# Performance work log

Hardware: AMD Instinct MI355X
Metric: run time of the kernel (lower is better)

Reference implementation:

```python
import jax, jax.numpy as jnp
import numpy as np

B, N, D, H = 4, 2048, 1024, 16
HD = D // H

def setup_inputs() -> dict:
    key = jax.random.key(0)
    ks = jax.random.split(key, 5)
    s = 0.02
    return {
        "x": jax.random.normal(ks[0], (B, N, D), dtype=jnp.float32),
        "W_qkv": jax.random.normal(ks[1], (D, 3 * D), dtype=jnp.float32) * s,
        "b_qkv": jnp.zeros((3 * D,), dtype=jnp.float32),
        "W_proj": jax.random.normal(ks[2], (D, D), dtype=jnp.float32) * s,
        "b_proj": jnp.zeros((D,), dtype=jnp.float32),
    }

def reference(x, W_qkv, b_qkv, W_proj, b_proj):
    scale = HD ** -0.5
    qkv = x @ W_qkv + b_qkv                       # [B,N,3D]
    qkv = qkv.reshape(B, N, 3, H, HD).transpose(2, 0, 3, 1, 4)  # [3,B,H,N,hd]
    q, k, v = qkv[0], qkv[1], qkv[2]
    attn = jnp.einsum('bhqd,bhkd->bhqk', q, k) * scale
    attn = jax.nn.softmax(attn, axis=-1)
    out = jnp.einsum('bhqk,bhkd->bhqd', attn, v)  # [B,H,N,hd]
    out = out.transpose(0, 2, 1, 3).reshape(B, N, D)
    return out @ W_proj + b_proj
```

## Files before the change

kernel.cpp:

```cpp
#include <hip/hip_runtime.h>


typedef __bf16 bf8v  __attribute__((ext_vector_type(8)));
typedef __bf16 bf4v  __attribute__((ext_vector_type(4)));
typedef float  f32x4 __attribute__((ext_vector_type(4)));

typedef const __attribute__((address_space(1))) void* gptr_t;
typedef __attribute__((address_space(3))) void*       lptr_t;

#define GLL16(g, l) __builtin_amdgcn_global_load_lds((gptr_t)(g), (lptr_t)(l), 16, 0, 0)

#define MFMA_BF16_16x16x32 __builtin_amdgcn_mfma_f32_16x16x32_bf16

static constexpr int Bsz = 4, Nseq = 2048, Dmod = 1024, H = 16, HD = 64;
static constexpr int Mtok = Bsz * Nseq;

__global__ __launch_bounds__(256) void cast_f32_bf16(const float* __restrict__ in,
                                                     __bf16* __restrict__ out, int n4) {
    int i = blockIdx.x * blockDim.x + threadIdx.x;
    int stride = gridDim.x * blockDim.x;
    for (; i < n4; i += stride) {
        float4 f = reinterpret_cast<const float4*>(in)[i];
        bf4v o;
        o[0] = (__bf16)f.x; o[1] = (__bf16)f.y; o[2] = (__bf16)f.z; o[3] = (__bf16)f.w;
        reinterpret_cast<bf4v*>(out)[i] = o;
    }
}

__global__ __launch_bounds__(256) void transpose_cast(const float* __restrict__ W,
                                                      __bf16* __restrict__ WT,
                                                      int K, int N) {
    __shared__ float t[32][33];
    int tx = threadIdx.x, ty = threadIdx.y;
    int bx = blockIdx.x, by = blockIdx.y;
#pragma unroll
    for (int j = 0; j < 4; ++j) {
        int k = by * 32 + ty + j * 8;
        int n = bx * 32 + tx;
        t[ty + j * 8][tx] = W[(size_t)k * N + n];
    }
    __syncthreads();
#pragma unroll
    for (int j = 0; j < 4; ++j) {
        int n = bx * 32 + ty + j * 8;
        int k = by * 32 + tx;
        WT[(size_t)n * K + k] = (__bf16)t[tx][ty + j * 8];
    }
}

template <int EPI>
__global__ __launch_bounds__(256) void gemm_bt(const __bf16* __restrict__ A,
                                               const __bf16* __restrict__ Bt,
                                               const float* __restrict__ bias,
                                               float* __restrict__ Cf,
                                               __bf16* __restrict__ Qo,
                                               __bf16* __restrict__ Ko,
                                               __bf16* __restrict__ Vo,
                                               int M, int N, int K) {
    __shared__ __attribute__((aligned(16))) __bf16 As[128 * 32];
    __shared__ __attribute__((aligned(16))) __bf16 Bs[128 * 32];

    const int nwg = gridDim.x;
    const int wg = (blockIdx.x & 7) * (nwg >> 3) + (blockIdx.x >> 3);

    const int nbn = N >> 7;
    const int bm = wg / nbn, bn = wg % nbn;
    const int tid = threadIdx.x;
    const int w = tid >> 6, l = tid & 63;
    const int wr = w >> 1, wc = w & 1;

    const int lr = l >> 2;
    const int lk = (l & 3) * 8;
    const int fr = l & 15;
    const int fk = (l >> 4) * 8;

    f32x4 acc[4][4] = {};

    for (int k0 = 0; k0 < K; k0 += 32) {
        const int c0 = w, c1 = w + 4;
        GLL16(A  + (size_t)(bm * 128 + c0 * 16 + lr) * K + k0 + lk, &As[c0 * 512]);
        GLL16(A  + (size_t)(bm * 128 + c1 * 16 + lr) * K + k0 + lk, &As[c1 * 512]);
        GLL16(Bt + (size_t)(bn * 128 + c0 * 16 + lr) * K + k0 + lk, &Bs[c0 * 512]);
        GLL16(Bt + (size_t)(bn * 128 + c1 * 16 + lr) * K + k0 + lk, &Bs[c1 * 512]);
        __syncthreads();

        bf8v af[4], bf[4];
#pragma unroll
        for (int m = 0; m < 4; ++m)
            af[m] = *(const bf8v*)&As[(wr * 64 + m * 16 + fr) * 32 + fk];
#pragma unroll
        for (int n = 0; n < 4; ++n)
            bf[n] = *(const bf8v*)&Bs[(wc * 64 + n * 16 + fr) * 32 + fk];
#pragma unroll
        for (int m = 0; m < 4; ++m)
#pragma unroll
            for (int n = 0; n < 4; ++n)
                acc[m][n] = MFMA_BF16_16x16x32(af[m], bf[n], acc[m][n], 0, 0, 0);
        __syncthreads();
    }

    const int r0 = bm * 128 + wr * 64;
    const int c0 = bn * 128 + wc * 64;
#pragma unroll
    for (int m = 0; m < 4; ++m)
#pragma unroll
        for (int n = 0; n < 4; ++n)
#pragma unroll
            for (int r = 0; r < 4; ++r) {
                int row = r0 + m * 16 + (l >> 4) * 4 + r;
                int col = c0 + n * 16 + (l & 15);
                float v = acc[m][n][r] + bias[col];
                if (EPI == 0) {
                    int mat = col >> 10, rem = col & 1023;
                    int h = rem >> 6, hd = rem & 63;
                    int b = row >> 11, nt = row & 2047;
                    size_t dst = (((size_t)(b * H + h)) * Nseq + nt) * HD + hd;
                    __bf16 val = (__bf16)v;
                    if (mat == 0)      Qo[dst] = val;
                    else if (mat == 1) Ko[dst] = val;
                    else               Vo[dst] = val;
                } else {
                    Cf[(size_t)row * N + col] = v;
                }
            }
}

__global__ __launch_bounds__(256) void attn_kernel(const __bf16* __restrict__ Q,
                                                   const __bf16* __restrict__ K,
                                                   const __bf16* __restrict__ V,
                                                   __bf16* __restrict__ Ao) {
    __shared__ __attribute__((aligned(16))) __bf16 Ks[64 * 64];
    __shared__ __attribute__((aligned(16))) __bf16 Vt[64 * 72];
    __shared__ __attribute__((aligned(16))) __bf16 Pl[4][16 * 72];

    const int tid = threadIdx.x;
    const int w = tid >> 6, l = tid & 63;

    const int nwg = gridDim.x;
    const int id = (blockIdx.x & 7) * (nwg >> 3) + (blockIdx.x >> 3);
    const int qb = id & 31;
    const int h = (id >> 5) & 15;
    const int b = id >> 9;
    const size_t base = (size_t)(b * H + h) * Nseq * HD;

    const int fr = l & 15;
    const int fkh = (l >> 4) * 8;

    const int qrow = qb * 64 + w * 16 + fr;
    bf8v qf[2];
    qf[0] = *(const bf8v*)&Q[base + (size_t)qrow * HD + fkh];
    qf[1] = *(const bf8v*)&Q[base + (size_t)qrow * HD + 32 + fkh];
#pragma unroll
    for (int j = 0; j < 8; ++j) {
        qf[0][j] = (__bf16)((float)qf[0][j] * 0.125f);
        qf[1][j] = (__bf16)((float)qf[1][j] * 0.125f);
    }

    f32x4 o[4] = {};
    float psum[4] = {0.f, 0.f, 0.f, 0.f};

    for (int kt = 0; kt < Nseq / 64; ++kt) {
        __syncthreads();
#pragma unroll
        for (int i = 0; i < 2; ++i) {
            int c = i * 256 + tid;
            int r = c >> 3, part = c & 7;
            GLL16(K + base + (size_t)(kt * 64 + r) * HD + ((part ^ (r & 7)) << 3),
                  &Ks[(i * 256 + w * 64) * 8]);
        }
#pragma unroll
        for (int i = 0; i < 2; ++i) {
            int c = i * 256 + tid;
            int rowk = c >> 3, part = c & 7;
            bf8v v8 = *(const bf8v*)&V[base + (size_t)(kt * 64 + rowk) * HD + part * 8];
#pragma unroll
            for (int j = 0; j < 8; ++j) {
                int d = part * 8 + j;
                Vt[d * 72 + (rowk ^ (part << 3))] = v8[j];
            }
        }
        __syncthreads();

        f32x4 s[4];
#pragma unroll
        for (int st = 0; st < 4; ++st) {
            int krow = st * 16 + fr;
            int key = (krow & 7) << 3;
            bf8v kf0 = *(const bf8v*)&Ks[krow * 64 + (fkh ^ key)];
            bf8v kf1 = *(const bf8v*)&Ks[krow * 64 + ((fkh + 32) ^ key)];
            f32x4 a = {};
            a = MFMA_BF16_16x16x32(qf[0], kf0, a, 0, 0, 0);
            a = MFMA_BF16_16x16x32(qf[1], kf1, a, 0, 0, 0);
            s[st] = a;
        }

        float p[4][4];
#pragma unroll
        for (int st = 0; st < 4; ++st)
#pragma unroll
            for (int r = 0; r < 4; ++r) p[st][r] = __expf(s[st][r]);
#pragma unroll
        for (int r = 0; r < 4; ++r)
            psum[r] += (p[0][r] + p[1][r]) + (p[2][r] + p[3][r]);

#pragma unroll
        for (int st = 0; st < 4; ++st)
#pragma unroll
            for (int r = 0; r < 4; ++r) {
                int qr = (l >> 4) * 4 + r;
                int col = st * 16 + (l & 15);
                Pl[w][qr * 72 + (col ^ ((qr >> 2) << 3))] = (__bf16)p[st][r];
            }

        int pkey = (fr >> 2) << 3;
        bf8v pa0 = *(const bf8v*)&Pl[w][fr * 72 + (fkh ^ pkey)];
        bf8v pa1 = *(const bf8v*)&Pl[w][fr * 72 + ((fkh + 32) ^ pkey)];
#pragma unroll
        for (int t = 0; t < 4; ++t) {
            int drow = t * 16 + fr;
            int vkey = ((drow >> 3) & 7) << 3;
            bf8v vf0 = *(const bf8v*)&Vt[drow * 72 + (fkh ^ vkey)];
            bf8v vf1 = *(const bf8v*)&Vt[drow * 72 + ((fkh + 32) ^ vkey)];
            o[t] = MFMA_BF16_16x16x32(pa0, vf0, o[t], 0, 0, 0);
            o[t] = MFMA_BF16_16x16x32(pa1, vf1, o[t], 0, 0, 0);
        }
    }

    float inv[4];
#pragma unroll
    for (int r = 0; r < 4; ++r) {
        float ps = psum[r];
#pragma unroll
        for (int off = 1; off < 16; off <<= 1) ps += __shfl_xor(ps, off);
        inv[r] = 1.f / ps;
    }
#pragma unroll
    for (int t = 0; t < 4; ++t)
#pragma unroll
        for (int r = 0; r < 4; ++r) {
            int row = (l >> 4) * 4 + r;
            int nq = qb * 64 + w * 16 + row;
            int hd = t * 16 + (l & 15);
            Ao[((size_t)(b * Nseq + nq)) * Dmod + h * HD + hd] = (__bf16)(o[t][r] * inv[r]);
        }
}

extern "C" void kernel_launch(void* const* d_in, const int* in_sizes, int n_in,
                              void* d_out, int out_size, void* d_ws, size_t ws_size,
                              hipStream_t stream) {
    const float* x      = (const float*)d_in[0];
    const float* W_qkv  = (const float*)d_in[1];
    const float* b_qkv  = (const float*)d_in[2];
    const float* W_proj = (const float*)d_in[3];
    const float* b_proj = (const float*)d_in[4];
    float* out = (float*)d_out;

    char* ws = (char*)d_ws;
    __bf16* Xb     = (__bf16*)(ws);
    __bf16* WqkvT  = (__bf16*)(ws + 16777216);
    __bf16* WprojT = (__bf16*)(ws + 16777216 + 6291456);
    __bf16* Qb     = (__bf16*)(ws + 25165824);
    __bf16* Kb     = (__bf16*)(ws + 25165824 + 16777216);
    __bf16* Vb     = (__bf16*)(ws + 25165824 + 33554432);
    __bf16* Ab     = Xb;

    cast_f32_bf16<<<2048, 256, 0, stream>>>(x, Xb, Mtok * Dmod / 4);

    dim3 tb(32, 8);
    transpose_cast<<<dim3(3 * Dmod / 32, Dmod / 32), tb, 0, stream>>>(W_qkv, WqkvT, Dmod, 3 * Dmod);
    transpose_cast<<<dim3(Dmod / 32, Dmod / 32), tb, 0, stream>>>(W_proj, WprojT, Dmod, Dmod);

    gemm_bt<0><<<(Mtok / 128) * (3 * Dmod / 128), 256, 0, stream>>>(
        Xb, WqkvT, b_qkv, nullptr, Qb, Kb, Vb, Mtok, 3 * Dmod, Dmod);

    attn_kernel<<<Bsz * H * (Nseq / 64), 256, 0, stream>>>(Qb, Kb, Vb, Ab);

    gemm_bt<1><<<(Mtok / 128) * (Dmod / 128), 256, 0, stream>>>(
        Ab, WprojT, b_proj, out, nullptr, nullptr, nullptr, Mtok, Dmod, Dmod);
}
```

Baseline: 331.6 us.

## Write V transposed from QKV GEMM and double-buffer attention K/V tiles

The QKV GEMM epilogue now writes V in a head-dim-major (transposed) layout, so the attention kernel can load V tiles with direct global-to-LDS copies instead of an in-register scatter transpose. K and V tiles are double-buffered, with the next tile prefetched while the current one is computed, and waits use vmcnt plus raw barriers. Each workgroup now handles 128 query rows (32 per wave) so every K/V fragment read from LDS feeds twice as many MFMAs. In exchange the GEMM's V stores become strided along the sequence, which may hurt that epilogue, and the grid shrinks to half as many workgroups.

```diff
diff --git a/kernel.cpp b/kernel.cpp
--- a/kernel.cpp
+++ b/kernel.cpp
@@ -114,135 +114,155 @@
                     int mat = col >> 10, rem = col & 1023;
                     int h = rem >> 6, hd = rem & 63;
                     int b = row >> 11, nt = row & 2047;
-                    size_t dst = (((size_t)(b * H + h)) * Nseq + nt) * HD + hd;
                     __bf16 val = (__bf16)v;
-                    if (mat == 0)      Qo[dst] = val;
-                    else if (mat == 1) Ko[dst] = val;
-                    else               Vo[dst] = val;
+                    if (mat == 0)
+                        Qo[(((size_t)(b * H + h)) * Nseq + nt) * HD + hd] = val;
+                    else if (mat == 1)
+                        Ko[(((size_t)(b * H + h)) * Nseq + nt) * HD + hd] = val;
+                    else
+                        Vo[(((size_t)(b * H + h)) * HD + hd) * Nseq + nt] = val;
                 } else {
                     Cf[(size_t)row * N + col] = v;
                 }
             }
 }
 
-__global__ __launch_bounds__(256) void attn_kernel(const __bf16* __restrict__ Q,
-                                                   const __bf16* __restrict__ K,
-                                                   const __bf16* __restrict__ V,
-                                                   __bf16* __restrict__ Ao) {
-    __shared__ __attribute__((aligned(16))) __bf16 Ks[64 * 64];
-    __shared__ __attribute__((aligned(16))) __bf16 Vt[64 * 72];
-    __shared__ __attribute__((aligned(16))) __bf16 Pl[4][16 * 72];
+__global__ __launch_bounds__(256, 2) void attn_kernel(const __bf16* __restrict__ Q,
+                                                      const __bf16* __restrict__ K,
+                                                      const __bf16* __restrict__ VT,
+                                                      __bf16* __restrict__ Ao) {
+    __shared__ __attribute__((aligned(16))) __bf16 Ks[2][64 * 64];
+    __shared__ __attribute__((aligned(16))) __bf16 Vts[2][64 * 64];
+    __shared__ __attribute__((aligned(16))) __bf16 Pl[4][32 * 72];
 
     const int tid = threadIdx.x;
     const int w = tid >> 6, l = tid & 63;
 
     const int nwg = gridDim.x;
     const int id = (blockIdx.x & 7) * (nwg >> 3) + (blockIdx.x >> 3);
-    const int qb = id & 31;
-    const int h = (id >> 5) & 15;
-    const int b = id >> 9;
+    const int qb = id & 15;
+    const int h = (id >> 4) & 15;
+    const int b = id >> 8;
     const size_t base = (size_t)(b * H + h) * Nseq * HD;
 
     const int fr = l & 15;
     const int fkh = (l >> 4) * 8;
 
-    const int qrow = qb * 64 + w * 16 + fr;
-    bf8v qf[2];
-    qf[0] = *(const bf8v*)&Q[base + (size_t)qrow * HD + fkh];
-    qf[1] = *(const bf8v*)&Q[base + (size_t)qrow * HD + 32 + fkh];
-#pragma unroll
-    for (int j = 0; j < 8; ++j) {
-        qf[0][j] = (__bf16)((float)qf[0][j] * 0.125f);
-        qf[1][j] = (__bf16)((float)qf[1][j] * 0.125f);
-    }
-
-    f32x4 o[4] = {};
-    float psum[4] = {0.f, 0.f, 0.f, 0.f};
+    const int sr0 = tid >> 3, sp0 = tid & 7;
+    const int sr1 = (256 + tid) >> 3, sp1 = tid & 7;
+
+    bf8v qf[2][2];
+#pragma unroll
+    for (int m = 0; m < 2; ++m) {
+        const int qrow = qb * 128 + w * 32 + m * 16 + fr;
+        qf[m][0] = *(const bf8v*)&Q[base + (size_t)qrow * HD + fkh];
+        qf[m][1] = *(const bf8v*)&Q[base + (size_t)qrow * HD + 32 + fkh];
+#pragma unroll
+        for (int j = 0; j < 8; ++j) {
+            qf[m][0][j] = (__bf16)((float)qf[m][0][j] * 0.125f);
+            qf[m][1][j] = (__bf16)((float)qf[m][1][j] * 0.125f);
+        }
+    }
+
+    f32x4 o[2][4] = {};
+    f32x4 psum[2] = {};
+
+#define STAGE(buf, kt)                                                                   \
+    do {                                                                                 \
+        GLL16(K  + base + (size_t)((kt) * 64 + sr0) * HD + ((sp0 ^ (sr0 & 7)) << 3),     \
+              &Ks[buf][(w * 64) * 8]);                                                   \
+        GLL16(K  + base + (size_t)((kt) * 64 + sr1) * HD + ((sp1 ^ (sr1 & 7)) << 3),     \
+              &Ks[buf][(256 + w * 64) * 8]);                                             \
+        GLL16(VT + base + (size_t)sr0 * Nseq + (kt) * 64 + ((sp0 ^ (sr0 & 7)) << 3),     \
+              &Vts[buf][(w * 64) * 8]);                                                  \
+        GLL16(VT + base + (size_t)sr1 * Nseq + (kt) * 64 + ((sp1 ^ (sr1 & 7)) << 3),     \
+              &Vts[buf][(256 + w * 64) * 8]);                                            \
+    } while (0)
+
+    STAGE(0, 0);
 
     for (int kt = 0; kt < Nseq / 64; ++kt) {
-        __syncthreads();
-#pragma unroll
-        for (int i = 0; i < 2; ++i) {
-            int c = i * 256 + tid;
-            int r = c >> 3, part = c & 7;
-            GLL16(K + base + (size_t)(kt * 64 + r) * HD + ((part ^ (r & 7)) << 3),
-                  &Ks[(i * 256 + w * 64) * 8]);
-        }
-#pragma unroll
-        for (int i = 0; i < 2; ++i) {
-            int c = i * 256 + tid;
-            int rowk = c >> 3, part = c & 7;
-            bf8v v8 = *(const bf8v*)&V[base + (size_t)(kt * 64 + rowk) * HD + part * 8];
-#pragma unroll
-            for (int j = 0; j < 8; ++j) {
-                int d = part * 8 + j;
-                Vt[d * 72 + (rowk ^ (part << 3))] = v8[j];
+        const int cur = kt & 1;
+        if (kt < Nseq / 64 - 1) {
+            STAGE(cur ^ 1, kt + 1);
+            asm volatile("s_waitcnt vmcnt(4)" ::: "memory");
+        } else {
+            asm volatile("s_waitcnt vmcnt(0)" ::: "memory");
+        }
+        __builtin_amdgcn_s_barrier();
+
+        f32x4 s[2][4];
+#pragma unroll
+        for (int st = 0; st < 4; ++st) {
+            const int krow = st * 16 + fr;
+            const int key = (fr & 7) << 3;
+            bf8v kf0 = *(const bf8v*)&Ks[cur][krow * 64 + (fkh ^ key)];
+            bf8v kf1 = *(const bf8v*)&Ks[cur][krow * 64 + ((fkh + 32) ^ key)];
+#pragma unroll
+            for (int m = 0; m < 2; ++m) {
+                f32x4 a = {};
+                a = MFMA_BF16_16x16x32(qf[m][0], kf0, a, 0, 0, 0);
+                a = MFMA_BF16_16x16x32(qf[m][1], kf1, a, 0, 0, 0);
+                s[m][st] = a;
             }
         }
-        __syncthreads();
-
-        f32x4 s[4];
-#pragma unroll
-        for (int st = 0; st < 4; ++st) {
-            int krow = st * 16 + fr;
-            int key = (krow & 7) << 3;
-            bf8v kf0 = *(const bf8v*)&Ks[krow * 64 + (fkh ^ key)];
-            bf8v kf1 = *(const bf8v*)&Ks[krow * 64 + ((fkh + 32) ^ key)];
-            f32x4 a = {};
-            a = MFMA_BF16_16x16x32(qf[0], kf0, a, 0, 0, 0);
-            a = MFMA_BF16_16x16x32(qf[1], kf1, a, 0, 0, 0);
-            s[st] = a;
-        }
-
-        float p[4][4];
-#pragma unroll
-        for (int st = 0; st < 4; ++st)
-#pragma unroll
-            for (int r = 0; r < 4; ++r) p[st][r] = __expf(s[st][r]);
-#pragma unroll
-        for (int r = 0; r < 4; ++r)
-            psum[r] += (p[0][r] + p[1][r]) + (p[2][r] + p[3][r]);
-
-#pragma unroll
-        for (int st = 0; st < 4; ++st)
+
+#pragma unroll
+        for (int m = 0; m < 2; ++m)
+#pragma unroll
+            for (int st = 0; st < 4; ++st)
+#pragma unroll
+                for (int r = 0; r < 4; ++r) {
+                    float p = __expf(s[m][st][r]);
+                    psum[m][r] += p;
+                    const int qr = m * 16 + (l >> 4) * 4 + r;
+                    Pl[w][qr * 72 + st * 16 + (l & 15)] = (__bf16)p;
+                }
+
+        bf8v pa[2][2];
+#pragma unroll
+        for (int m = 0; m < 2; ++m) {
+            const int prow = m * 16 + fr;
+            pa[m][0] = *(const bf8v*)&Pl[w][prow * 72 + fkh];
+            pa[m][1] = *(const bf8v*)&Pl[w][prow * 72 + 32 + fkh];
+        }
+#pragma unroll
+        for (int t = 0; t < 4; ++t) {
+            const int drow = t * 16 + fr;
+            const int key = (fr & 7) << 3;
+            bf8v vf0 = *(const bf8v*)&Vts[cur][drow * 64 + (fkh ^ key)];
+            bf8v vf1 = *(const bf8v*)&Vts[cur][drow * 64 + ((fkh + 32) ^ key)];
+#pragma unroll
+            for (int m = 0; m < 2; ++m) {
+                o[m][t] = MFMA_BF16_16x16x32(pa[m][0], vf0, o[m][t], 0, 0, 0);
+                o[m][t] = MFMA_BF16_16x16x32(pa[m][1], vf1, o[m][t], 0, 0, 0);
+            }
+        }
+        __builtin_amdgcn_s_barrier();
+    }
+#undef STAGE
+
+#pragma unroll
+    for (int m = 0; m < 2; ++m)
+#pragma unroll
+        for (int r = 0; r < 4; ++r) {
+            float ps = psum[m][r];
+#pragma unroll
+            for (int off = 1; off < 16; off <<= 1) ps += __shfl_xor(ps, off);
+            psum[m][r] = 1.f / ps;
+        }
+#pragma unroll
+    for (int m = 0; m < 2; ++m)
+#pragma unroll
+        for (int t = 0; t < 4; ++t)
 #pragma unroll
             for (int r = 0; r < 4; ++r) {
-                int qr = (l >> 4) * 4 + r;
-                int col = st * 16 + (l & 15);
-                Pl[w][qr * 72 + (col ^ ((qr >> 2) << 3))] = (__bf16)p[st][r];
+                const int row = m * 16 + (l >> 4) * 4 + r;
+                const int nq = qb * 128 + w * 32 + row;
+                const int hd = t * 16 + (l & 15);
+                Ao[((size_t)(b * Nseq + nq)) * Dmod + h * HD + hd] =
+                    (__bf16)(o[m][t][r] * psum[m][r]);
             }
-
-        int pkey = (fr >> 2) << 3;
-        bf8v pa0 = *(const bf8v*)&Pl[w][fr * 72 + (fkh ^ pkey)];
-        bf8v pa1 = *(const bf8v*)&Pl[w][fr * 72 + ((fkh + 32) ^ pkey)];
-#pragma unroll
-        for (int t = 0; t < 4; ++t) {
-            int drow = t * 16 + fr;
-            int vkey = ((drow >> 3) & 7) << 3;
-            bf8v vf0 = *(const bf8v*)&Vt[drow * 72 + (fkh ^ vkey)];
-            bf8v vf1 = *(const bf8v*)&Vt[drow * 72 + ((fkh + 32) ^ vkey)];
-            o[t] = MFMA_BF16_16x16x32(pa0, vf0, o[t], 0, 0, 0);
-            o[t] = MFMA_BF16_16x16x32(pa1, vf1, o[t], 0, 0, 0);
-        }
-    }
-
-    float inv[4];
-#pragma unroll
-    for (int r = 0; r < 4; ++r) {
-        float ps = psum[r];
-#pragma unroll
-        for (int off = 1; off < 16; off <<= 1) ps += __shfl_xor(ps, off);
-        inv[r] = 1.f / ps;
-    }
-#pragma unroll
-    for (int t = 0; t < 4; ++t)
-#pragma unroll
-        for (int r = 0; r < 4; ++r) {
-            int row = (l >> 4) * 4 + r;
-            int nq = qb * 64 + w * 16 + row;
-            int hd = t * 16 + (l & 15);
-            Ao[((size_t)(b * Nseq + nq)) * Dmod + h * HD + hd] = (__bf16)(o[t][r] * inv[r]);
-        }
 }
 
 extern "C" void kernel_launch(void* const* d_in, const int* in_sizes, int n_in,
@@ -261,7 +281,7 @@
     __bf16* WprojT = (__bf16*)(ws + 16777216 + 6291456);
     __bf16* Qb     = (__bf16*)(ws + 25165824);
     __bf16* Kb     = (__bf16*)(ws + 25165824 + 16777216);
-    __bf16* Vb     = (__bf16*)(ws + 25165824 + 33554432);
+    __bf16* VTb    = (__bf16*)(ws + 25165824 + 33554432);
     __bf16* Ab     = Xb;
 
     cast_f32_bf16<<<2048, 256, 0, stream>>>(x, Xb, Mtok * Dmod / 4);
@@ -271,9 +291,9 @@
     transpose_cast<<<dim3(Dmod / 32, Dmod / 32), tb, 0, stream>>>(W_proj, WprojT, Dmod, Dmod);
 
     gemm_bt<0><<<(Mtok / 128) * (3 * Dmod / 128), 256, 0, stream>>>(
-        Xb, WqkvT, b_qkv, nullptr, Qb, Kb, Vb, Mtok, 3 * Dmod, Dmod);
-
-    attn_kernel<<<Bsz * H * (Nseq / 64), 256, 0, stream>>>(Qb, Kb, Vb, Ab);
+        Xb, WqkvT, b_qkv, nullptr, Qb, Kb, VTb, Mtok, 3 * Dmod, Dmod);
+
+    attn_kernel<<<Bsz * H * (Nseq / 128), 256, 0, stream>>>(Qb, Kb, VTb, Ab);
 
     gemm_bt<1><<<(Mtok / 128) * (Dmod / 128), 256, 0, stream>>>(
         Ab, WprojT, b_proj, out, nullptr, nullptr, nullptr, Mtok, Dmod, Dmod);
```

Result: slower. 340.6 us (+2.7%).
